# Optimization experiments

Hardware: AMD Instinct MI355X
Metric: run time of the kernel (lower is better)

## Reference

```python
import jax, jax.numpy as jnp
import numpy as np

N_NODES = 131072          # total nodes across all expressions
NODES_PER_EXPR = 64       # nodes per expression (left or right side)
NUM_SEG = N_NODES // NODES_PER_EXPR   # 2048 segments = 1024 equations x 2 sides
VOCAB = 320
D_MODEL = 128
NUM_LAYERS = 4


def setup_inputs() -> dict:
    key = jax.random.key(0)
    ks = jax.random.split(key, 8)
    # combined-vocab index per node (leaf->token id, internal->function id + offset)
    node_idx = jax.random.randint(ks[0], (N_NODES,), 0, VOCAB)
    # 4 incoming edges per node: left child, right child, parent, self.
    # index N_NODES is the padding node (zero features).
    nb = jax.random.randint(ks[1], (N_NODES, 3), 0, N_NODES + 1)
    self_col = jnp.arange(N_NODES)[:, None]
    neighbors = jnp.concatenate([nb, self_col], axis=1)  # [N, 4]
    # contiguous expression segments (matches batched DGL graph layout)
    seg_ids = jnp.arange(N_NODES) // NODES_PER_EXPR
    emb = jax.random.normal(ks[2], (VOCAB, D_MODEL), dtype=jnp.float32) * 0.02
    W0 = jax.random.normal(ks[3], (NUM_LAYERS, 4 * D_MODEL, D_MODEL), dtype=jnp.float32) * (1.0 / np.sqrt(4 * D_MODEL))
    b0 = jnp.zeros((NUM_LAYERS, D_MODEL), dtype=jnp.float32)
    W1 = jax.random.normal(ks[4], (NUM_LAYERS, D_MODEL, D_MODEL), dtype=jnp.float32) * (1.0 / np.sqrt(D_MODEL))
    b1 = jnp.zeros((NUM_LAYERS, D_MODEL), dtype=jnp.float32)
    out_bias = jnp.zeros((1,), dtype=jnp.float32)
    return {"node_idx": node_idx, "neighbors": neighbors, "seg_ids": seg_ids,
            "emb": emb, "W0": W0, "b0": b0, "W1": W1, "b1": b1, "out_bias": out_bias}


def reference(node_idx, neighbors, seg_ids, emb, W0, b0, W1, b1, out_bias):
    N, d = node_idx.shape[0], emb.shape[1]
    feats = emb[node_idx]                                   # [N, d] embedding lookup
    num_layers = W0.shape[0]
    for l in range(num_layers):
        # padding node (id N) always contributes zero features
        f_pad = jnp.concatenate([feats, jnp.zeros((1, d), feats.dtype)], axis=0)
        gathered = f_pad[neighbors].reshape(N, 4 * d)       # [N, 4d] mailbox gather+flatten
        h = jax.nn.relu(gathered @ W0[l] + b0[l])           # FunctionModule layer 1
        feats = h @ W1[l] + b1[l]                           # FunctionModule layer 2
    # per-expression mean feature (graph readout)
    sums = jax.ops.segment_sum(feats, seg_ids, num_segments=NUM_SEG)      # [2B, d]
    cnts = jax.ops.segment_sum(jnp.ones((N,), feats.dtype), seg_ids, num_segments=NUM_SEG)
    means = sums / cnts[:, None]
    means = means.reshape(-1, 2, d)                         # [B, 2, d] (left, right)
    logits = jnp.einsum('bd,bd->b', means[:, 0], means[:, 1]) + out_bias[0]
    return logits
```

## Files before the change

kernel.cpp:

```cpp
#include <hip/hip_runtime.h>

#define N_NODES 131072
#define D 128
#define NLAYERS 4
#define AS_STRIDE 136

typedef _Float16 f16;
typedef _Float16 f16x8 __attribute__((ext_vector_type(8)));
typedef _Float16 f16x4 __attribute__((ext_vector_type(4)));
typedef float f32x4 __attribute__((ext_vector_type(4)));

__global__ __launch_bounds__(256) void prep_weights(
    const float* __restrict__ W0, const float* __restrict__ W1,
    f16* __restrict__ W0t, f16* __restrict__ W1t)
{
    __shared__ float T[64][65];
    int b = blockIdx.x;
    const float* src; f16* dst; int K, tk, tn;
    if (b < 64) {
        int l = b >> 4; tk = (b >> 1) & 7; tn = b & 1;
        src = W0 + (size_t)l * 512 * 128; dst = W0t + (size_t)l * 128 * 512; K = 512;
    } else {
        int bb = b - 64; int l = bb >> 2; tk = (bb >> 1) & 1; tn = bb & 1;
        src = W1 + (size_t)l * 128 * 128; dst = W1t + (size_t)l * 128 * 128; K = 128;
    }
    const int tid = threadIdx.x;
#pragma unroll
    for (int i = 0; i < 16; ++i) {
        int u = tid + 256 * i;
        int kk = u >> 6, nn = u & 63;
        T[kk][nn] = src[(size_t)(tk * 64 + kk) * 128 + tn * 64 + nn];
    }
    __syncthreads();
#pragma unroll
    for (int i = 0; i < 16; ++i) {
        int u = tid + 256 * i;
        int nn = u >> 6, kk = u & 63;
        dst[(size_t)(tn * 64 + nn) * K + tk * 64 + kk] = (f16)T[kk][nn];
    }
}

__global__ __launch_bounds__(256) void embed_f16(
    const int* __restrict__ node_idx, const float* __restrict__ emb,
    f16* __restrict__ fa, f16* __restrict__ fb)
{
    const int tid = threadIdx.x;
    if (blockIdx.x == 16384) {
        if (tid < 32) {
            f16x8 z = {0, 0, 0, 0, 0, 0, 0, 0};
            f16* base = (tid >> 4) ? fb : fa;
            *(f16x8*)&base[(size_t)N_NODES * D + (tid & 15) * 8] = z;
        }
        return;
    }
    int i = blockIdx.x * 256 + tid;
    int v = i >> 5, c = i & 31;
    int tok = node_idx[v];
    float4 x = ((const float4*)emb)[(size_t)tok * 32 + c];
    f16x4 y = { (f16)x.x, (f16)x.y, (f16)x.z, (f16)x.w };
    *(f16x4*)&fa[(size_t)v * D + c * 4] = y;
}

__global__ __launch_bounds__(256, 2) void layer_fused(
    const f16* __restrict__ fin, f16* __restrict__ fout,
    const int* __restrict__ neighbors,
    const f16* __restrict__ W0t, const float* __restrict__ b0,
    const f16* __restrict__ W1t, const float* __restrict__ b1)
{
    __shared__ f16 As[128][AS_STRIDE];
    __shared__ f16 Bs[128][AS_STRIDE];
    __shared__ int nbr_s[512];

    const int tid  = threadIdx.x;
    const int bm   = blockIdx.x * 128;
    const int lane = tid & 63;
    const int wave = tid >> 6;
    const int wr = wave >> 1, wc = wave & 1;
    const int quad = lane >> 4, lm = lane & 15;
    const int seg = tid & 15, r0 = tid >> 4;

    nbr_s[tid]       = neighbors[bm * 4 + tid];
    nbr_s[tid + 256] = neighbors[bm * 4 + 256 + tid];

    float bb0[4], bb1[4];
#pragma unroll
    for (int c = 0; c < 4; ++c) {
        bb0[c] = b0[wc * 64 + c * 16 + lm];
        bb1[c] = b1[wc * 64 + c * 16 + lm];
    }

    f16x8 ra[8], rb[8];
    __syncthreads();

#pragma unroll
    for (int i = 0; i < 8; ++i) {
        int row = r0 + 16 * i;
        int nbr = nbr_s[row * 4 + 0];
        ra[i] = *(const f16x8*)&fin[(size_t)nbr * D + seg * 8];
        rb[i] = *(const f16x8*)&W0t[(size_t)row * 512 + seg * 8];
    }
#pragma unroll
    for (int i = 0; i < 8; ++i) {
        int row = r0 + 16 * i;
        *(f16x8*)&As[row][seg * 8] = ra[i];
        *(f16x8*)&Bs[row][seg * 8] = rb[i];
    }
    __syncthreads();

    f32x4 acc1[4][4];
#pragma unroll
    for (int r = 0; r < 4; ++r)
#pragma unroll
        for (int c = 0; c < 4; ++c) acc1[r][c] = (f32x4){0.f, 0.f, 0.f, 0.f};

    for (int e = 0; e < 4; ++e) {
        if (e < 3) {
#pragma unroll
            for (int i = 0; i < 8; ++i) {
                int row = r0 + 16 * i;
                int nbr = nbr_s[row * 4 + e + 1];
                ra[i] = *(const f16x8*)&fin[(size_t)nbr * D + seg * 8];
                rb[i] = *(const f16x8*)&W0t[(size_t)row * 512 + (e + 1) * 128 + seg * 8];
            }
        } else {
#pragma unroll
            for (int i = 0; i < 8; ++i) {
                int row = r0 + 16 * i;
                rb[i] = *(const f16x8*)&W1t[(size_t)row * 128 + seg * 8];
            }
        }
#pragma unroll
        for (int t = 0; t < 4; ++t) {
            const int k0 = t * 32 + quad * 8;
            f16x8 af[4], bf[4];
#pragma unroll
            for (int r = 0; r < 4; ++r)
                af[r] = *(const f16x8*)&As[wr * 64 + r * 16 + lm][k0];
#pragma unroll
            for (int c = 0; c < 4; ++c)
                bf[c] = *(const f16x8*)&Bs[wc * 64 + c * 16 + lm][k0];
#pragma unroll
            for (int r = 0; r < 4; ++r)
#pragma unroll
                for (int c = 0; c < 4; ++c)
                    acc1[r][c] = __builtin_amdgcn_mfma_f32_16x16x32_f16(
                        af[r], bf[c], acc1[r][c], 0, 0, 0);
        }
        __syncthreads();
        if (e < 3) {
#pragma unroll
            for (int i = 0; i < 8; ++i) {
                int row = r0 + 16 * i;
                *(f16x8*)&As[row][seg * 8] = ra[i];
                *(f16x8*)&Bs[row][seg * 8] = rb[i];
            }
            __syncthreads();
        }
    }

    unsigned int hpk[4][4][2];
#pragma unroll
    for (int c = 0; c < 4; ++c) {
#pragma unroll
        for (int r = 0; r < 4; ++r) {
#pragma unroll
            for (int p = 0; p < 2; ++p) {
                float v0 = fmaxf(acc1[r][c][2 * p]     + bb0[c], 0.f);
                float v1 = fmaxf(acc1[r][c][2 * p + 1] + bb0[c], 0.f);
                unsigned short u0 = __builtin_bit_cast(unsigned short, (f16)v0);
                unsigned short u1 = __builtin_bit_cast(unsigned short, (f16)v1);
                hpk[r][c][p] = ((unsigned)u1 << 16) | u0;
            }
        }
    }

#pragma unroll
    for (int r = 0; r < 4; ++r)
#pragma unroll
        for (int c = 0; c < 4; ++c) {
            int gcol = wc * 64 + c * 16 + lm;
#pragma unroll
            for (int reg = 0; reg < 4; ++reg) {
                int grow = wr * 64 + r * 16 + quad * 4 + reg;
                unsigned pk = hpk[r][c][reg >> 1];
                unsigned short bits = (reg & 1) ? (unsigned short)(pk >> 16)
                                                : (unsigned short)(pk & 0xffff);
                As[grow][gcol] = __builtin_bit_cast(f16, bits);
            }
        }
#pragma unroll
    for (int i = 0; i < 8; ++i) {
        int row = r0 + 16 * i;
        *(f16x8*)&Bs[row][seg * 8] = rb[i];
    }
    __syncthreads();

    f32x4 acc2[4][4];
#pragma unroll
    for (int r = 0; r < 4; ++r)
#pragma unroll
        for (int c = 0; c < 4; ++c) acc2[r][c] = (f32x4){0.f, 0.f, 0.f, 0.f};

#pragma unroll
    for (int t = 0; t < 4; ++t) {
        const int k0 = t * 32 + quad * 8;
        f16x8 af[4], bf[4];
#pragma unroll
        for (int r = 0; r < 4; ++r)
            af[r] = *(const f16x8*)&As[wr * 64 + r * 16 + lm][k0];
#pragma unroll
        for (int c = 0; c < 4; ++c)
            bf[c] = *(const f16x8*)&Bs[wc * 64 + c * 16 + lm][k0];
#pragma unroll
        for (int r = 0; r < 4; ++r)
#pragma unroll
            for (int c = 0; c < 4; ++c)
                acc2[r][c] = __builtin_amdgcn_mfma_f32_16x16x32_f16(
                    af[r], bf[c], acc2[r][c], 0, 0, 0);
    }
    __syncthreads();

#pragma unroll
    for (int r = 0; r < 4; ++r)
#pragma unroll
        for (int c = 0; c < 4; ++c) {
            int gcol = wc * 64 + c * 16 + lm;
#pragma unroll
            for (int reg = 0; reg < 4; ++reg) {
                int grow = wr * 64 + r * 16 + quad * 4 + reg;
                As[grow][gcol] = (f16)(acc2[r][c][reg] + bb1[c]);
            }
        }
    __syncthreads();
#pragma unroll
    for (int i = 0; i < 8; ++i) {
        int row = r0 + 16 * i;
        *(f16x8*)&fout[(size_t)(bm + row) * D + seg * 8] =
            *(const f16x8*)&As[row][seg * 8];
    }
}

__global__ __launch_bounds__(256) void readout_f16(
    const f16* __restrict__ feats, const float* __restrict__ out_bias,
    float* __restrict__ logits)
{
    __shared__ float ms[2][128];
    const int b   = blockIdx.x;
    const int tid = threadIdx.x;
    const int side = tid >> 7, d = tid & 127;

    const f16* base = feats + ((size_t)b * 128 + side * 64) * D + d;
    float s = 0.f;
#pragma unroll 8
    for (int n = 0; n < 64; ++n) s += (float)base[(size_t)n * D];
    ms[side][d] = s * (1.0f / 64.0f);
    __syncthreads();

    if (tid < 64) {
        float v = ms[0][tid] * ms[1][tid] + ms[0][tid + 64] * ms[1][tid + 64];
#pragma unroll
        for (int off = 32; off; off >>= 1) v += __shfl_down(v, off);
        if (tid == 0) logits[b] = v + out_bias[0];
    }
}

extern "C" void kernel_launch(void* const* d_in, const int* in_sizes, int n_in,
                              void* d_out, int out_size, void* d_ws, size_t ws_size,
                              hipStream_t stream) {
    const int*   node_idx  = (const int*)d_in[0];
    const int*   neighbors = (const int*)d_in[1];
    const float* emb       = (const float*)d_in[3];
    const float* W0        = (const float*)d_in[4];
    const float* b0        = (const float*)d_in[5];
    const float* W1        = (const float*)d_in[6];
    const float* b1        = (const float*)d_in[7];
    const float* out_bias  = (const float*)d_in[8];
    float*       logits    = (float*)d_out;

    const size_t NP1 = (size_t)N_NODES + 1;
    f16* feats_a = (f16*)d_ws;
    f16* feats_b = feats_a + NP1 * D;
    f16* W0t     = feats_b + NP1 * D;
    f16* W1t     = W0t + (size_t)NLAYERS * 512 * 128;

    prep_weights<<<80, 256, 0, stream>>>(W0, W1, W0t, W1t);
    embed_f16<<<16385, 256, 0, stream>>>(node_idx, emb, feats_a, feats_b);

    f16* fin = feats_a; f16* fout = feats_b;
    for (int l = 0; l < NLAYERS; ++l) {
        layer_fused<<<N_NODES / 128, 256, 0, stream>>>(
            fin, fout, neighbors,
            W0t + (size_t)l * 512 * 128, b0 + (size_t)l * 128,
            W1t + (size_t)l * 128 * 128, b1 + (size_t)l * 128);
        f16* t = fin; fin = fout; fout = t;
    }
    readout_f16<<<N_NODES / 128, 256, 0, stream>>>(feats_a, out_bias, logits);
}
```

Baseline: 244.8 us.

## Use LDS DMA gather, swizzled LDS, direct-global weights, and fold embedding into layer 0

Replaces the register-staged gather with global_load_lds DMA into one XOR-swizzled LDS tile, reads weight fragments straight from global or L2 instead of staging them in LDS, and halves LDS use so occupancy can rise to 4 blocks per CU. The embedding kernel is removed: neighbour indices are remapped to token ids so layer 0 gathers directly from a converted fp16 embedding table, and the padding-row zeroing moves into prep_weights. This removes the per-node embedding materialisation and some LDS traffic, but adds a token-remap pass and leans on cache locality for the weight reads.

Result: slower. 384.5 us (+57.0%).

```diff
diff --git a/kernel.cpp b/kernel.cpp
--- a/kernel.cpp
+++ b/kernel.cpp
@@ -3,19 +3,35 @@
 #define N_NODES 131072
 #define D 128
 #define NLAYERS 4
-#define AS_STRIDE 136
+#define VOCAB 320
 
 typedef _Float16 f16;
 typedef _Float16 f16x8 __attribute__((ext_vector_type(8)));
-typedef _Float16 f16x4 __attribute__((ext_vector_type(4)));
 typedef float f32x4 __attribute__((ext_vector_type(4)));
+typedef unsigned int u32;
+
+__device__ __forceinline__ void lds_dma16(f16* lds, const f16* g) {
+    __builtin_amdgcn_global_load_lds(
+        (const __attribute__((address_space(1))) u32*)(const void*)g,
+        (__attribute__((address_space(3))) u32*)(void*)lds, 16, 0, 0);
+}
 
 __global__ __launch_bounds__(256) void prep_weights(
     const float* __restrict__ W0, const float* __restrict__ W1,
-    f16* __restrict__ W0t, f16* __restrict__ W1t)
+    f16* __restrict__ W0t, f16* __restrict__ W1t,
+    f16* __restrict__ fa, f16* __restrict__ fb)
 {
     __shared__ float T[64][65];
     int b = blockIdx.x;
+    const int tid = threadIdx.x;
+    if (b == 80) {
+        if (tid < 32) {
+            f16x8 z = {0, 0, 0, 0, 0, 0, 0, 0};
+            f16* base = (tid >> 4) ? fb : fa;
+            *(f16x8*)&base[(size_t)N_NODES * D + (tid & 15) * 8] = z;
+        }
+        return;
+    }
     const float* src; f16* dst; int K, tk, tn;
     if (b < 64) {
         int l = b >> 4; tk = (b >> 1) & 7; tn = b & 1;
@@ -24,7 +40,6 @@
         int bb = b - 64; int l = bb >> 2; tk = (bb >> 1) & 1; tn = bb & 1;
         src = W1 + (size_t)l * 128 * 128; dst = W1t + (size_t)l * 128 * 128; K = 128;
     }
-    const int tid = threadIdx.x;
 #pragma unroll
     for (int i = 0; i < 16; ++i) {
         int u = tid + 256 * i;
@@ -40,35 +55,71 @@
     }
 }
 
-__global__ __launch_bounds__(256) void embed_f16(
-    const int* __restrict__ node_idx, const float* __restrict__ emb,
-    f16* __restrict__ fa, f16* __restrict__ fb)
+__global__ __launch_bounds__(256) void prep_emb(
+    const float* __restrict__ emb, f16* __restrict__ embP)
 {
     const int tid = threadIdx.x;
-    if (blockIdx.x == 16384) {
-        if (tid < 32) {
+    if (blockIdx.x == 40) {
+        if (tid < 16) {
             f16x8 z = {0, 0, 0, 0, 0, 0, 0, 0};
-            f16* base = (tid >> 4) ? fb : fa;
-            *(f16x8*)&base[(size_t)N_NODES * D + (tid & 15) * 8] = z;
+            *(f16x8*)&embP[(size_t)VOCAB * D + tid * 8] = z;
         }
         return;
     }
     int i = blockIdx.x * 256 + tid;
-    int v = i >> 5, c = i & 31;
-    int tok = node_idx[v];
-    float4 x = ((const float4*)emb)[(size_t)tok * 32 + c];
-    f16x4 y = { (f16)x.x, (f16)x.y, (f16)x.z, (f16)x.w };
-    *(f16x4*)&fa[(size_t)v * D + c * 4] = y;
-}
-
-__global__ __launch_bounds__(256, 2) void layer_fused(
+    int t = i >> 5, c = i & 31;
+    float4 x = ((const float4*)emb)[(size_t)t * 32 + c];
+    f16 y0 = (f16)x.x, y1 = (f16)x.y, y2 = (f16)x.z, y3 = (f16)x.w;
+    f16 v[4] = {y0, y1, y2, y3};
+    *(unsigned long long*)&embP[(size_t)t * D + c * 4] = *(unsigned long long*)v;
+}
+
+__global__ __launch_bounds__(256) void prep_nbrtok(
+    const int* __restrict__ node_idx, const int* __restrict__ neighbors,
+    int* __restrict__ nbr_tok)
+{
+    int i = blockIdx.x * 256 + threadIdx.x;
+    int nbr = neighbors[i];
+    nbr_tok[i] = (nbr < N_NODES) ? node_idx[nbr] : VOCAB;
+}
+
+#define MFMA_STAGE(ACC, WP, WSTRIDE)                                          \
+    {                                                                         \
+        f16x8 bfc[4], bfn[4];                                                 \
+        _Pragma("unroll")                                                     \
+        for (int c = 0; c < 4; ++c)                                           \
+            bfc[c] = *(const f16x8*)&(WP)[(size_t)(wc*64 + c*16 + lm) * (WSTRIDE) + quad*8]; \
+        __syncthreads();                                                      \
+        _Pragma("unroll")                                                     \
+        for (int t = 0; t < 4; ++t) {                                         \
+            if (t < 3) {                                                      \
+                _Pragma("unroll")                                             \
+                for (int c = 0; c < 4; ++c)                                   \
+                    bfn[c] = *(const f16x8*)&(WP)[(size_t)(wc*64 + c*16 + lm) * (WSTRIDE) + (t+1)*32 + quad*8]; \
+            }                                                                 \
+            f16x8 af[4];                                                      \
+            _Pragma("unroll")                                                 \
+            for (int r = 0; r < 4; ++r) {                                     \
+                int row = wr*64 + r*16 + lm;                                  \
+                af[r] = *(const f16x8*)&As[row*128 + (((4*t + quad) ^ (lm & 7)) * 8)]; \
+            }                                                                 \
+            _Pragma("unroll")                                                 \
+            for (int r = 0; r < 4; ++r)                                       \
+                _Pragma("unroll")                                             \
+                for (int c = 0; c < 4; ++c)                                   \
+                    ACC[r][c] = __builtin_amdgcn_mfma_f32_16x16x32_f16(af[r], bfc[c], ACC[r][c], 0, 0, 0); \
+            _Pragma("unroll")                                                 \
+            for (int c = 0; c < 4; ++c) bfc[c] = bfn[c];                      \
+        }                                                                     \
+    }
+
+__global__ __launch_bounds__(256, 4) void layer_fused(
     const f16* __restrict__ fin, f16* __restrict__ fout,
-    const int* __restrict__ neighbors,
+    const int* __restrict__ nbrtab,
     const f16* __restrict__ W0t, const float* __restrict__ b0,
     const f16* __restrict__ W1t, const float* __restrict__ b1)
 {
-    __shared__ f16 As[128][AS_STRIDE];
-    __shared__ f16 Bs[128][AS_STRIDE];
+    __shared__ f16 As[128 * 128];
     __shared__ int nbr_s[512];
 
     const int tid  = threadIdx.x;
@@ -77,101 +128,52 @@
     const int wave = tid >> 6;
     const int wr = wave >> 1, wc = wave & 1;
     const int quad = lane >> 4, lm = lane & 15;
-    const int seg = tid & 15, r0 = tid >> 4;
-
-    nbr_s[tid]       = neighbors[bm * 4 + tid];
-    nbr_s[tid + 256] = neighbors[bm * 4 + 256 + tid];
-
-    float bb0[4], bb1[4];
+    const int seg  = tid & 15;
+    const int r0   = tid >> 4;
+    const int kb   = seg ^ (r0 & 7);
+
+    nbr_s[tid]       = nbrtab[bm * 4 + tid];
+    nbr_s[tid + 256] = nbrtab[bm * 4 + 256 + tid];
+    __syncthreads();
+
+    int rn[8];
+#pragma unroll
+    for (int i = 0; i < 8; ++i) rn[i] = nbr_s[(r0 + 16 * i) * 4];
+
+    f32x4 acc1[4][4];
+#pragma unroll
+    for (int r = 0; r < 4; ++r)
+#pragma unroll
+        for (int c = 0; c < 4; ++c) acc1[r][c] = (f32x4){0.f, 0.f, 0.f, 0.f};
+
+#pragma unroll 1
+    for (int e = 0; e < 4; ++e) {
+#pragma unroll
+        for (int i = 0; i < 8; ++i)
+            lds_dma16(&As[(4 * wave + 16 * i) * 128],
+                      fin + (size_t)rn[i] * D + kb * 8);
+        if (e < 3) {
+#pragma unroll
+            for (int i = 0; i < 8; ++i) rn[i] = nbr_s[(r0 + 16 * i) * 4 + e + 1];
+        }
+        MFMA_STAGE(acc1, W0t + (size_t)e * 128, 512)
+        __syncthreads();
+    }
+
+    unsigned int hpk[4][4][2];
 #pragma unroll
     for (int c = 0; c < 4; ++c) {
-        bb0[c] = b0[wc * 64 + c * 16 + lm];
-        bb1[c] = b1[wc * 64 + c * 16 + lm];
-    }
-
-    f16x8 ra[8], rb[8];
-    __syncthreads();
-
-#pragma unroll
-    for (int i = 0; i < 8; ++i) {
-        int row = r0 + 16 * i;
-        int nbr = nbr_s[row * 4 + 0];
-        ra[i] = *(const f16x8*)&fin[(size_t)nbr * D + seg * 8];
-        rb[i] = *(const f16x8*)&W0t[(size_t)row * 512 + seg * 8];
-    }
-#pragma unroll
-    for (int i = 0; i < 8; ++i) {
-        int row = r0 + 16 * i;
-        *(f16x8*)&As[row][seg * 8] = ra[i];
-        *(f16x8*)&Bs[row][seg * 8] = rb[i];
-    }
-    __syncthreads();
-
-    f32x4 acc1[4][4];
-#pragma unroll
-    for (int r = 0; r < 4; ++r)
-#pragma unroll
-        for (int c = 0; c < 4; ++c) acc1[r][c] = (f32x4){0.f, 0.f, 0.f, 0.f};
-
-    for (int e = 0; e < 4; ++e) {
-        if (e < 3) {
-#pragma unroll
-            for (int i = 0; i < 8; ++i) {
-                int row = r0 + 16 * i;
-                int nbr = nbr_s[row * 4 + e + 1];
-                ra[i] = *(const f16x8*)&fin[(size_t)nbr * D + seg * 8];
-                rb[i] = *(const f16x8*)&W0t[(size_t)row * 512 + (e + 1) * 128 + seg * 8];
-            }
-        } else {
-#pragma unroll
-            for (int i = 0; i < 8; ++i) {
-                int row = r0 + 16 * i;
-                rb[i] = *(const f16x8*)&W1t[(size_t)row * 128 + seg * 8];
-            }
-        }
-#pragma unroll
-        for (int t = 0; t < 4; ++t) {
-            const int k0 = t * 32 + quad * 8;
-            f16x8 af[4], bf[4];
-#pragma unroll
-            for (int r = 0; r < 4; ++r)
-                af[r] = *(const f16x8*)&As[wr * 64 + r * 16 + lm][k0];
-#pragma unroll
-            for (int c = 0; c < 4; ++c)
-                bf[c] = *(const f16x8*)&Bs[wc * 64 + c * 16 + lm][k0];
-#pragma unroll
-            for (int r = 0; r < 4; ++r)
-#pragma unroll
-                for (int c = 0; c < 4; ++c)
-                    acc1[r][c] = __builtin_amdgcn_mfma_f32_16x16x32_f16(
-                        af[r], bf[c], acc1[r][c], 0, 0, 0);
-        }
-        __syncthreads();
-        if (e < 3) {
-#pragma unroll
-            for (int i = 0; i < 8; ++i) {
-                int row = r0 + 16 * i;
-                *(f16x8*)&As[row][seg * 8] = ra[i];
-                *(f16x8*)&Bs[row][seg * 8] = rb[i];
-            }
-            __syncthreads();
-        }
-    }
-
-    unsigned int hpk[4][4][2];
-#pragma unroll
-    for (int c = 0; c < 4; ++c) {
-#pragma unroll
-        for (int r = 0; r < 4; ++r) {
+        float b0v = b0[wc * 64 + c * 16 + lm];
+#pragma unroll
+        for (int r = 0; r < 4; ++r)
 #pragma unroll
             for (int p = 0; p < 2; ++p) {
-                float v0 = fmaxf(acc1[r][c][2 * p]     + bb0[c], 0.f);
-                float v1 = fmaxf(acc1[r][c][2 * p + 1] + bb0[c], 0.f);
+                float v0 = fmaxf(acc1[r][c][2 * p]     + b0v, 0.f);
+                float v1 = fmaxf(acc1[r][c][2 * p + 1] + b0v, 0.f);
                 unsigned short u0 = __builtin_bit_cast(unsigned short, (f16)v0);
                 unsigned short u1 = __builtin_bit_cast(unsigned short, (f16)v1);
-                hpk[r][c][p] = ((unsigned)u1 << 16) | u0;
+                hpk[r][c][p] = ((u32)u1 << 16) | u0;
             }
-        }
     }
 
 #pragma unroll
@@ -179,21 +181,17 @@
 #pragma unroll
         for (int c = 0; c < 4; ++c) {
             int gcol = wc * 64 + c * 16 + lm;
+            int blk = gcol >> 3, el = gcol & 7;
 #pragma unroll
             for (int reg = 0; reg < 4; ++reg) {
                 int grow = wr * 64 + r * 16 + quad * 4 + reg;
                 unsigned pk = hpk[r][c][reg >> 1];
                 unsigned short bits = (reg & 1) ? (unsigned short)(pk >> 16)
                                                 : (unsigned short)(pk & 0xffff);
-                As[grow][gcol] = __builtin_bit_cast(f16, bits);
+                As[grow * 128 + ((blk ^ (grow & 7)) * 8) + el] =
+                    __builtin_bit_cast(f16, bits);
             }
         }
-#pragma unroll
-    for (int i = 0; i < 8; ++i) {
-        int row = r0 + 16 * i;
-        *(f16x8*)&Bs[row][seg * 8] = rb[i];
-    }
-    __syncthreads();
 
     f32x4 acc2[4][4];
 #pragma unroll
@@ -201,34 +199,21 @@
 #pragma unroll
         for (int c = 0; c < 4; ++c) acc2[r][c] = (f32x4){0.f, 0.f, 0.f, 0.f};
 
-#pragma unroll
-    for (int t = 0; t < 4; ++t) {
-        const int k0 = t * 32 + quad * 8;
-        f16x8 af[4], bf[4];
-#pragma unroll
-        for (int r = 0; r < 4; ++r)
-            af[r] = *(const f16x8*)&As[wr * 64 + r * 16 + lm][k0];
-#pragma unroll
-        for (int c = 0; c < 4; ++c)
-            bf[c] = *(const f16x8*)&Bs[wc * 64 + c * 16 + lm][k0];
-#pragma unroll
-        for (int r = 0; r < 4; ++r)
-#pragma unroll
-            for (int c = 0; c < 4; ++c)
-                acc2[r][c] = __builtin_amdgcn_mfma_f32_16x16x32_f16(
-                    af[r], bf[c], acc2[r][c], 0, 0, 0);
-    }
+    MFMA_STAGE(acc2, W1t, 128)
     __syncthreads();
 
 #pragma unroll
     for (int r = 0; r < 4; ++r)
 #pragma unroll
         for (int c = 0; c < 4; ++c) {
+            float b1v = b1[wc * 64 + c * 16 + lm];
             int gcol = wc * 64 + c * 16 + lm;
+            int blk = gcol >> 3, el = gcol & 7;
 #pragma unroll
             for (int reg = 0; reg < 4; ++reg) {
                 int grow = wr * 64 + r * 16 + quad * 4 + reg;
-                As[grow][gcol] = (f16)(acc2[r][c][reg] + bb1[c]);
+                As[grow * 128 + ((blk ^ (grow & 7)) * 8) + el] =
+                    (f16)(acc2[r][c][reg] + b1v);
             }
         }
     __syncthreads();
@@ -236,7 +221,7 @@
     for (int i = 0; i < 8; ++i) {
         int row = r0 + 16 * i;
         *(f16x8*)&fout[(size_t)(bm + row) * D + seg * 8] =
-            *(const f16x8*)&As[row][seg * 8];
+            *(const f16x8*)&As[row * 128 + kb * 8];
     }
 }
 
@@ -282,17 +267,23 @@
     f16* feats_b = feats_a + NP1 * D;
     f16* W0t     = feats_b + NP1 * D;
     f16* W1t     = W0t + (size_t)NLAYERS * 512 * 128;
-
-    prep_weights<<<80, 256, 0, stream>>>(W0, W1, W0t, W1t);
-    embed_f16<<<16385, 256, 0, stream>>>(node_idx, emb, feats_a, feats_b);
+    f16* embP    = W1t + (size_t)NLAYERS * 128 * 128;
+    int* nbr_tok = (int*)(embP + (size_t)(VOCAB + 1) * D);
+
+    prep_weights<<<81, 256, 0, stream>>>(W0, W1, W0t, W1t, feats_a, feats_b);
+    prep_emb<<<41, 256, 0, stream>>>(emb, embP);
+    prep_nbrtok<<<N_NODES * 4 / 256, 256, 0, stream>>>(node_idx, neighbors, nbr_tok);
+
+    layer_fused<<<N_NODES / 128, 256, 0, stream>>>(
+        embP, feats_a, nbr_tok, W0t, b0, W1t, b1);
 
     f16* fin = feats_a; f16* fout = feats_b;
-    for (int l = 0; l < NLAYERS; ++l) {
+    for (int l = 1; l < NLAYERS; ++l) {
         layer_fused<<<N_NODES / 128, 256, 0, stream>>>(
             fin, fout, neighbors,
             W0t + (size_t)l * 512 * 128, b0 + (size_t)l * 128,
             W1t + (size_t)l * 128 * 128, b1 + (size_t)l * 128);
         f16* t = fin; fin = fout; fout = t;
     }
-    readout_f16<<<N_NODES / 128, 256, 0, stream>>>(feats_a, out_bias, logits);
-}
+    readout_f16<<<N_NODES / 128, 256, 0, stream>>>(feats_b, out_bias, logits);
+}
```
